# Kernel tuning notes

Hardware: AMD Instinct MI355X
Metric: run time of the kernel (lower is better)

Reference implementation:

```python
import jax, jax.numpy as jnp
import numpy as np

B, N, C = 4, 2048, 384
H = 6
D = C // H
HID = int(C * 4.0)
EPS = 1e-5


def setup_inputs() -> dict:
    key = jax.random.key(0)
    ks = jax.random.split(key, 12)
    s = lambda fan_in: 1.0 / np.sqrt(fan_in)
    return {
        "x": jax.random.normal(ks[0], (B, N, C), dtype=jnp.float32),
        "ln1_g": jnp.ones((C,), jnp.float32),
        "ln1_b": jnp.zeros((C,), jnp.float32),
        "w_qkv": jax.random.uniform(ks[1], (C, 3 * C), jnp.float32, -s(C), s(C)),
        "w_proj": jax.random.uniform(ks[2], (C, C), jnp.float32, -s(C), s(C)),
        "b_proj": jax.random.uniform(ks[3], (C,), jnp.float32, -s(C), s(C)),
        "ln2_g": jnp.ones((C,), jnp.float32),
        "ln2_b": jnp.zeros((C,), jnp.float32),
        "w_fc1": jax.random.uniform(ks[4], (C, HID), jnp.float32, -s(C), s(C)),
        "b_fc1": jax.random.uniform(ks[5], (HID,), jnp.float32, -s(C), s(C)),
        "w_fc2": jax.random.uniform(ks[6], (HID, C), jnp.float32, -s(HID), s(HID)),
        "b_fc2": jax.random.uniform(ks[7], (C,), jnp.float32, -s(HID), s(HID)),
    }


def _layernorm(x, g, b):
    mu = jnp.mean(x, axis=-1, keepdims=True)
    var = jnp.mean(jnp.square(x - mu), axis=-1, keepdims=True)
    return (x - mu) * jax.lax.rsqrt(var + EPS) * g + b


def reference(x, ln1_g, ln1_b, w_qkv, w_proj, b_proj, ln2_g, ln2_b, w_fc1, b_fc1, w_fc2, b_fc2):
    # --- attention branch (pre-norm) ---
    h = _layernorm(x, ln1_g, ln1_b)                       # [B,N,C]
    qkv = (h @ w_qkv).reshape(B, N, 3, H, D)
    q = jnp.transpose(qkv[:, :, 0], (0, 2, 1, 3))          # [B,H,N,D]
    k = jnp.transpose(qkv[:, :, 1], (0, 2, 1, 3))
    v = jnp.transpose(qkv[:, :, 2], (0, 2, 1, 3))
    scale = D ** -0.5
    attn = jnp.einsum("bhnd,bhmd->bhnm", q, k) * scale     # [B,H,N,N]
    attn = jax.nn.softmax(attn, axis=-1)
    o = jnp.einsum("bhnm,bhmd->bhnd", attn, v)             # [B,H,N,D]
    o = jnp.transpose(o, (0, 2, 1, 3)).reshape(B, N, C)
    x = x + (o @ w_proj + b_proj)
    # --- MLP branch (pre-norm) ---
    h2 = _layernorm(x, ln2_g, ln2_b)
    m = jax.nn.gelu(h2 @ w_fc1 + b_fc1, approximate=False)  # torch nn.GELU = exact erf
    x = x + (m @ w_fc2 + b_fc2)
    return x
```

## Files before the change

### kernel.cpp

```cpp
#include <hip/hip_runtime.h>

typedef __bf16 bf16x8 __attribute__((ext_vector_type(8)));
typedef float f32x4 __attribute__((ext_vector_type(4)));
typedef float f32x16 __attribute__((ext_vector_type(16)));
typedef unsigned short u16;
typedef unsigned int u32;
typedef unsigned long long u64;

#define BB 4
#define NNCTX 2048
#define CCH 384
#define NHEAD 6
#define DHEAD 64
#define HIDDIM 1536

__device__ __forceinline__ u16 f2bf(float f){
  u32 u = __builtin_bit_cast(u32, f);
  u = u + 0x7fffu + ((u >> 16) & 1u);
  return (u16)(u >> 16);
}
__device__ __forceinline__ float bf2f(u16 h){
  u32 u = ((u32)h) << 16;
  return __builtin_bit_cast(float, u);
}

union U8 { uint4 u; u16 s[8]; bf16x8 v; };
union F8 { u32 w[4]; bf16x8 v; };

__global__ __launch_bounds__(256) void cast_tr(const float* __restrict__ w0, const float* __restrict__ w1,
    const float* __restrict__ w2, const float* __restrict__ w3,
    u16* __restrict__ o0, u16* __restrict__ o1, u16* __restrict__ o2, u16* __restrict__ o3){
  __shared__ float S[64][65];
  int idx = blockIdx.x;
  const float* src; u16* dst; int K, N, kt, nt;
  if (idx < 108){ src = w0; dst = o0; K = 384; N = 1152; kt = idx / 18; nt = idx % 18; }
  else if (idx < 144){ idx -= 108; src = w1; dst = o1; K = 384; N = 384; kt = idx / 6; nt = idx % 6; }
  else if (idx < 288){ idx -= 144; src = w2; dst = o2; K = 384; N = 1536; kt = idx / 24; nt = idx % 24; }
  else { idx -= 288; src = w3; dst = o3; K = 1536; N = 384; kt = idx / 6; nt = idx % 6; }
  int t = threadIdx.x;
  int r4 = t >> 6, c = t & 63;
  int k0 = kt * 64, n0 = nt * 64;
  #pragma unroll
  for (int i = 0; i < 16; i++){
    int row = i * 4 + r4;
    S[row][c] = src[(size_t)(k0 + row) * N + n0 + c];
  }
  __syncthreads();
  #pragma unroll
  for (int i = 0; i < 16; i++){
    int row = i * 4 + r4;
    dst[(size_t)(n0 + row) * K + k0 + c] = f2bf(S[c][row]);
  }
}

__global__ __launch_bounds__(128) void ln_kernel(const float* __restrict__ x, const float* __restrict__ g,
                                                 const float* __restrict__ bb, u16* __restrict__ out){
  int row = blockIdx.x, t = threadIdx.x;
  const float* xr = x + (size_t)row * CCH;
  float v0 = xr[t], v1 = xr[t + 128], v2 = xr[t + 256];
  float s = v0 + v1 + v2;
  float q = v0 * v0 + v1 * v1 + v2 * v2;
  #pragma unroll
  for (int o = 32; o; o >>= 1){ s += __shfl_down(s, o); q += __shfl_down(q, o); }
  __shared__ float sh[4];
  if ((t & 63) == 0){ int w = t >> 6; sh[w * 2] = s; sh[w * 2 + 1] = q; }
  __syncthreads();
  float sum = sh[0] + sh[2], ssq = sh[1] + sh[3];
  float mu = sum * (1.0f / 384.0f);
  float rstd = rsqrtf(ssq * (1.0f / 384.0f) - mu * mu + 1e-5f);
  size_t base = (size_t)row * CCH;
  out[base + t]       = f2bf((v0 - mu) * rstd * g[t]       + bb[t]);
  out[base + t + 128] = f2bf((v1 - mu) * rstd * g[t + 128] + bb[t + 128]);
  out[base + t + 256] = f2bf((v2 - mu) * rstd * g[t + 256] + bb[t + 256]);
}

template<int EPI, int DBUF>
__global__ __launch_bounds__(256) void gemm_bf16(const u16* __restrict__ A, const u16* __restrict__ Bt,
    int K, int Nn, u16* __restrict__ outb, const float* __restrict__ bias,
    const float* __restrict__ resid, float* __restrict__ outf)
{
  __shared__ u16 As[DBUF + 1][64][68];
  __shared__ u16 Bs[DBUF + 1][64][68];
  int t = threadIdx.x;
  int bm = blockIdx.y * 64, bn = blockIdx.x * 64;
  int l = t & 63, w = t >> 6;
  int wm = (w >> 1) * 32, wn = (w & 1) * 32;
  f32x4 acc[2][2] = {};
  int ar0 = t >> 3, ac0 = (t & 7) * 8;
  uint4 la0, la1, lb0, lb1;
  auto LOADG = [&](int k0){
    la0 = *(const uint4*)&A[(size_t)(bm + ar0) * K + k0 + ac0];
    la1 = *(const uint4*)&A[(size_t)(bm + ar0 + 32) * K + k0 + ac0];
    lb0 = *(const uint4*)&Bt[(size_t)(bn + ar0) * K + k0 + ac0];
    lb1 = *(const uint4*)&Bt[(size_t)(bn + ar0 + 32) * K + k0 + ac0];
  };
  auto WRITEL = [&](int bf){
    *(uint4*)&As[bf][ar0][ac0]      = la0;
    *(uint4*)&As[bf][ar0 + 32][ac0] = la1;
    *(uint4*)&Bs[bf][ar0][ac0]      = lb0;
    *(uint4*)&Bs[bf][ar0 + 32][ac0] = lb1;
  };
  auto COMPUTE = [&](int bf){
    #pragma unroll
    for (int ks = 0; ks < 2; ks++){
      int kb = ks * 32 + (l >> 4) * 8;
      bf16x8 a0  = *(const bf16x8*)&As[bf][wm + (l & 15)][kb];
      bf16x8 a1  = *(const bf16x8*)&As[bf][wm + 16 + (l & 15)][kb];
      bf16x8 bb0 = *(const bf16x8*)&Bs[bf][wn + (l & 15)][kb];
      bf16x8 bb1 = *(const bf16x8*)&Bs[bf][wn + 16 + (l & 15)][kb];
      acc[0][0] = __builtin_amdgcn_mfma_f32_16x16x32_bf16(a0, bb0, acc[0][0], 0, 0, 0);
      acc[0][1] = __builtin_amdgcn_mfma_f32_16x16x32_bf16(a0, bb1, acc[0][1], 0, 0, 0);
      acc[1][0] = __builtin_amdgcn_mfma_f32_16x16x32_bf16(a1, bb0, acc[1][0], 0, 0, 0);
      acc[1][1] = __builtin_amdgcn_mfma_f32_16x16x32_bf16(a1, bb1, acc[1][1], 0, 0, 0);
    }
  };
  if constexpr (DBUF){
    int nk = K >> 6;
    LOADG(0);
    WRITEL(0);
    __syncthreads();
    for (int ki = 0; ki < nk; ki++){
      int cur = ki & 1;
      if (ki + 1 < nk) LOADG((ki + 1) << 6);
      COMPUTE(cur);
      if (ki + 1 < nk) WRITEL(cur ^ 1);
      __syncthreads();
    }
  } else {
    for (int k0 = 0; k0 < K; k0 += 64){
      __syncthreads();
      LOADG(k0);
      WRITEL(0);
      __syncthreads();
      COMPUTE(0);
    }
  }
  if constexpr (EPI == 1){
    #pragma unroll
    for (int mi = 0; mi < 2; mi++)
    #pragma unroll
    for (int ni = 0; ni < 2; ni++)
    #pragma unroll
    for (int r = 0; r < 4; r++){
      int row = bm + wm + mi * 16 + ((l >> 4) << 2) + r;
      int col = bn + wn + ni * 16 + (l & 15);
      size_t idx = (size_t)row * Nn + col;
      outf[idx] = resid[idx] + acc[mi][ni][r] + bias[col];
    }
  } else {
    __syncthreads();
    u16 (*CS)[68] = As[0];
    #pragma unroll
    for (int mi = 0; mi < 2; mi++)
    #pragma unroll
    for (int ni = 0; ni < 2; ni++)
    #pragma unroll
    for (int r = 0; r < 4; r++){
      int row = wm + mi * 16 + ((l >> 4) << 2) + r;
      int col = wn + ni * 16 + (l & 15);
      float v = acc[mi][ni][r];
      if (EPI == 2){
        v += bias[bn + col];
        v = 0.5f * v * (1.0f + erff(v * 0.70710678118f));
      }
      CS[row][col] = f2bf(v);
    }
    __syncthreads();
    int row = t >> 2, c0 = (t & 3) * 16;
    uint4 v0 = *(const uint4*)&CS[row][c0];
    uint4 v1 = *(const uint4*)&CS[row][c0 + 8];
    u16* op = outb + (size_t)(bm + row) * Nn + bn + c0;
    *(uint4*)op       = v0;
    *(uint4*)(op + 8) = v1;
  }
}

#define PVSTEP(O0, O1, O2, O3, SX, BASE, VT)                                     \
  {                                                                              \
    float p0 = __builtin_exp2f(SX[BASE + 0] - m_q);                              \
    float p1 = __builtin_exp2f(SX[BASE + 1] - m_q);                              \
    float p2 = __builtin_exp2f(SX[BASE + 2] - m_q);                              \
    float p3 = __builtin_exp2f(SX[BASE + 3] - m_q);                              \
    float p4 = __builtin_exp2f(SX[BASE + 4] - m_q);                              \
    float p5 = __builtin_exp2f(SX[BASE + 5] - m_q);                              \
    float p6 = __builtin_exp2f(SX[BASE + 6] - m_q);                              \
    float p7 = __builtin_exp2f(SX[BASE + 7] - m_q);                              \
    u32 wa0, wa1, wb0, wb1;                                                      \
    asm("v_cvt_pk_bf16_f32 %0, %1, %2" : "=v"(wa0) : "v"(p0), "v"(p1));          \
    asm("v_cvt_pk_bf16_f32 %0, %1, %2" : "=v"(wa1) : "v"(p2), "v"(p3));          \
    asm("v_cvt_pk_bf16_f32 %0, %1, %2" : "=v"(wb0) : "v"(p4), "v"(p5));          \
    asm("v_cvt_pk_bf16_f32 %0, %1, %2" : "=v"(wb1) : "v"(p6), "v"(p7));          \
    asm("v_permlane32_swap_b32 %0, %1" : "+v"(wa0), "+v"(wb0));                  \
    asm("v_permlane32_swap_b32 %0, %1" : "+v"(wa1), "+v"(wb1));                  \
    F8 pa; pa.w[0] = wa0; pa.w[1] = wa1; pa.w[2] = wb0; pa.w[3] = wb1;           \
    u64 ta, tb, tc, td;                                                          \
    asm volatile("ds_read_b64_tr_b16 %0, %4 offset:" #O0 "\n\t"                  \
                 "ds_read_b64_tr_b16 %1, %4 offset:" #O1 "\n\t"                  \
                 "ds_read_b64_tr_b16 %2, %4 offset:" #O2 "\n\t"                  \
                 "ds_read_b64_tr_b16 %3, %4 offset:" #O3 "\n\t"                  \
                 "s_waitcnt lgkmcnt(0)"                                          \
                 : "=&v"(ta), "=&v"(tb), "=&v"(tc), "=&v"(td)                    \
                 : "v"(VT));                                                     \
    __builtin_amdgcn_sched_barrier(0);                                           \
    F8 f0, f1;                                                                   \
    f0.w[0] = (u32)ta; f0.w[1] = (u32)(ta >> 32);                                \
    f0.w[2] = (u32)tb; f0.w[3] = (u32)(tb >> 32);                                \
    f1.w[0] = (u32)tc; f1.w[1] = (u32)(tc >> 32);                                \
    f1.w[2] = (u32)td; f1.w[3] = (u32)(td >> 32);                                \
    l_acc = __builtin_amdgcn_mfma_f32_32x32x16_bf16(pa.v, onesf, l_acc, 0, 0, 0);\
    o_0 = __builtin_amdgcn_mfma_f32_32x32x16_bf16(pa.v, f0.v, o_0, 0, 0, 0);     \
    o_1 = __builtin_amdgcn_mfma_f32_32x32x16_bf16(pa.v, f1.v, o_1, 0, 0, 0);     \
  }

__global__ __launch_bounds__(256, 3) void attn_mfma(const u16* __restrict__ qkv,
    u16* __restrict__ o0buf, u16* __restrict__ o1buf, float2* __restrict__ mlbuf){
  __shared__ u16 Ks[2][64][68];
  __shared__ __attribute__((aligned(128))) u16 Vs[2][4096];
  int t = threadIdx.x;
  int w = t >> 6, l = t & 63;
  int c31 = l & 31, hi = l >> 5, hi8 = hi * 8;
  int id = blockIdx.x;
  int xcd = id & 7, slot = id >> 3;
  int qb = slot & 15;
  int group = (slot >> 4) * 8 + xcd;
  int bh = group % (BB * NHEAD);
  int sp = group / (BB * NHEAD);
  int b = bh / NHEAD, h = bh % NHEAD;
  int q0 = qb * 128;

  const float QS = 0.1803368801111716f;
  bf16x8 qf[4];
  {
    const u16* qp = qkv + (size_t)(b * NNCTX + q0 + w * 32 + c31) * 1152 + h * 64 + hi8;
    #pragma unroll
    for (int c = 0; c < 4; c++){
      U8 r; r.u = *(const uint4*)(qp + c * 16);
      #pragma unroll
      for (int j = 0; j < 8; j++) r.s[j] = f2bf(bf2f(r.s[j]) * QS);
      qf[c] = r.v;
    }
  }
  bf16x8 onesf;
  {
    U8 r;
    #pragma unroll
    for (int j = 0; j < 8; j++) r.s[j] = 0x3F80;
    onesf = r.v;
  }
  f32x16 o_0 = {}, o_1 = {};
  f32x16 l_acc = {};
  float m_q = -3.4e38f;

  const size_t kvrow = (size_t)(b * NNCTX) * 1152 + h * 64;
  int kkey = t >> 2, kdp = (t & 3) * 16;
  int vkey = t & 63, vdblk = w * 16;
  int voff = (vkey >> 2) * 256 + w * 64 + (vkey & 3) * 16;
  int lg = l >> 4, lr16 = l & 15;
  u32 vtr = (u32)(uintptr_t)(&Vs[0][0]) + (u32)((lg >> 1) * 1024 + (lg & 1) * 128 + lr16 * 8);

  int ktbeg = sp * 16, ktend = ktbeg + 16;
  const u16* kp = qkv + kvrow + (size_t)(ktbeg * 64 + kkey) * 1152 + 384 + kdp;
  const u16* vp = qkv + kvrow + (size_t)(ktbeg * 64 + vkey) * 1152 + 768 + vdblk;
  const int KVSTRIDE = 64 * 1152;

  uint4 kra, krb, vra, vrb;
  auto LOADT = [&](){
    kra = *(const uint4*)kp;
    krb = *(const uint4*)(kp + 8);
    vra = *(const uint4*)vp;
    vrb = *(const uint4*)(vp + 8);
    kp += KVSTRIDE; vp += KVSTRIDE;
  };
  auto WRITET = [&](int bf){
    *(uint4*)&Ks[bf][kkey][kdp]     = kra;
    *(uint4*)&Ks[bf][kkey][kdp + 8] = krb;
    *(uint4*)&Vs[bf][voff]     = vra;
    *(uint4*)&Vs[bf][voff + 8] = vrb;
  };

  LOADT();
  WRITET(0);
  __syncthreads();

  for (int kt = ktbeg; kt < ktend; kt++){
    int cur = (kt - ktbeg) & 1;
    if (kt + 1 < ktend) LOADT();

    f32x16 s0 = {}, s1 = {};
    #pragma unroll
    for (int c = 0; c < 4; c++){
      bf16x8 kf0 = *(const bf16x8*)&Ks[cur][c31][c * 16 + hi8];
      bf16x8 kf1 = *(const bf16x8*)&Ks[cur][32 + c31][c * 16 + hi8];
      s0 = __builtin_amdgcn_mfma_f32_32x32x16_bf16(kf0, qf[c], s0, 0, 0, 0);
      s1 = __builtin_amdgcn_mfma_f32_32x32x16_bf16(kf1, qf[c], s1, 0, 0, 0);
    }
    float tm[16];
    #pragma unroll
    for (int r = 0; r < 16; r++) tm[r] = fmaxf(s0[r], s1[r]);
    #pragma unroll
    for (int st = 8; st >= 1; st >>= 1)
      #pragma unroll
      for (int r = 0; r < st; r++) tm[r] = fmaxf(tm[r], tm[r + st]);
    float px = fmaxf(tm[0], __shfl_xor(tm[0], 32));
    if (!__all(px <= m_q + 8.f)){
      float mn = fmaxf(m_q, px);
      float a = __builtin_exp2f(m_q - mn);
      m_q = mn;
      #pragma unroll
      for (int r = 0; r < 16; r++){
        int cr = (r & 3) + 8 * (r >> 2) + 4 * hi;
        float ar = __shfl(a, cr);
        o_0[r] *= ar; o_1[r] *= ar; l_acc[r] *= ar;
      }
    }
    u32 vt = vtr + (u32)(cur * 8192);
    PVSTEP(0, 512, 256, 768, s0, 0, vt)
    PVSTEP(2048, 2560, 2304, 2816, s0, 8, vt)
    PVSTEP(4096, 4608, 4352, 4864, s1, 0, vt)
    PVSTEP(6144, 6656, 6400, 6912, s1, 8, vt)

    if (kt + 1 < ktend) WRITET(cur ^ 1);
    __syncthreads();
  }
  u16* obuf = sp ? o1buf : o0buf;
  #pragma unroll
  for (int r = 0; r < 16; r++){
    int cr = (r & 3) + 8 * (r >> 2) + 4 * hi;
    float mr = __shfl(m_q, cr);
    int n = q0 + w * 32 + cr;
    size_t row = (size_t)(b * NNCTX + n);
    u16* op = obuf + row * CCH + h * 64;
    op[c31]      = f2bf(o_0[r]);
    op[32 + c31] = f2bf(o_1[r]);
    if (c31 == 0)
      mlbuf[((size_t)(sp * BB * NHEAD + bh)) * NNCTX + n] = make_float2(mr, l_acc[r]);
  }
}

__global__ __launch_bounds__(256) void attn_combine(u16* __restrict__ o0, const u16* __restrict__ o1,
    const float2* __restrict__ ml){
  int g = blockIdx.x * 256 + threadIdx.x;
  int row = g / 48, c8 = g - row * 48;
  int head = c8 >> 3;
  int b = row >> 11, n = row & 2047;
  int bh = b * NHEAD + head;
  float2 a = ml[(size_t)bh * NNCTX + n];
  float2 c = ml[(size_t)(BB * NHEAD + bh) * NNCTX + n];
  float M = fmaxf(a.x, c.x);
  float e0 = exp2f(a.x - M), e1 = exp2f(c.x - M);
  float inv = 1.0f / (a.y * e0 + c.y * e1);
  float s0 = e0 * inv, s1 = e1 * inv;
  size_t idx = (size_t)row * CCH + c8 * 8;
  U8 x0, x1, o;
  x0.u = *(const uint4*)(o0 + idx);
  x1.u = *(const uint4*)(o1 + idx);
  #pragma unroll
  for (int j = 0; j < 8; j++) o.s[j] = f2bf(bf2f(x0.s[j]) * s0 + bf2f(x1.s[j]) * s1);
  *(uint4*)(o0 + idx) = o.u;
}

extern "C" void kernel_launch(void* const* d_in, const int* in_sizes, int n_in,
                              void* d_out, int out_size, void* d_ws, size_t ws_size,
                              hipStream_t stream){
  const float* x      = (const float*)d_in[0];
  const float* ln1_g  = (const float*)d_in[1];
  const float* ln1_b  = (const float*)d_in[2];
  const float* w_qkv  = (const float*)d_in[3];
  const float* w_proj = (const float*)d_in[4];
  const float* b_proj = (const float*)d_in[5];
  const float* ln2_g  = (const float*)d_in[6];
  const float* ln2_b  = (const float*)d_in[7];
  const float* w_fc1  = (const float*)d_in[8];
  const float* b_fc1  = (const float*)d_in[9];
  const float* w_fc2  = (const float*)d_in[10];
  const float* b_fc2  = (const float*)d_in[11];
  float* out = (float*)d_out;

  u16* ws = (u16*)d_ws;
  u16* wqkv_bf  = ws;
  u16* wproj_bf = wqkv_bf + 442368;
  u16* wfc1_bf  = wproj_bf + 147456;
  u16* wfc2_bf  = wfc1_bf + 589824;
  u16* h_bf     = wfc2_bf + 589824;
  u16* qkv_bf   = h_bf + 3145728;
  u16* opart1   = qkv_bf + 9437184;
  float2* mlbuf = (float2*)(opart1 + 3145728);
  u16* opart0   = h_bf;
  u16* m_bf     = qkv_bf;

  cast_tr<<<432, 256, 0, stream>>>(w_qkv, w_proj, w_fc1, w_fc2, wqkv_bf, wproj_bf, wfc1_bf, wfc2_bf);

  ln_kernel<<<8192, 128, 0, stream>>>(x, ln1_g, ln1_b, h_bf);
  gemm_bf16<0, 0><<<dim3(18, 128), 256, 0, stream>>>(h_bf, wqkv_bf, 384, 1152, qkv_bf, nullptr, nullptr, nullptr);
  attn_mfma<<<dim3(768), 256, 0, stream>>>(qkv_bf, opart0, opart1, mlbuf);
  attn_combine<<<1536, 256, 0, stream>>>(opart0, opart1, mlbuf);
  gemm_bf16<1, 1><<<dim3(6, 128), 256, 0, stream>>>(opart0, wproj_bf, 384, 384, nullptr, b_proj, x, out);
  ln_kernel<<<8192, 128, 0, stream>>>(out, ln2_g, ln2_b, h_bf);
  gemm_bf16<2, 0><<<dim3(24, 128), 256, 0, stream>>>(h_bf, wfc1_bf, 384, 1536, m_bf, b_fc1, nullptr, nullptr);
  gemm_bf16<1, 1><<<dim3(6, 128), 256, 0, stream>>>(m_bf, wfc2_bf, 1536, 384, nullptr, b_fc2, out, out);
}
```

Before: 155.9 us.

## Add 128x128-tile GEMM with direct global-to-LDS loads for QKV and FC1

Adds a new bf16 MFMA GEMM kernel that uses 128x128 output tiles, a 4x4 MFMA fragment grid per wave, and global_load_lds async copies into double-buffered shared memory. The QKV and FC1 GEMMs switch to it. The larger tiles raise operand reuse and cut global traffic per FLOP, and the direct-to-LDS loads skip staging through registers. The epilogue writes through LDS for coalesced 16-byte stores. Risks are fewer blocks, higher register pressure, and LDS bank conflicts on the unpadded 32-wide rows.

```diff
diff --git a/kernel.cpp b/kernel.cpp
--- a/kernel.cpp
+++ b/kernel.cpp
@@ -26,6 +26,11 @@
 
 union U8 { uint4 u; u16 s[8]; bf16x8 v; };
 union F8 { u32 w[4]; bf16x8 v; };
+
+__device__ __forceinline__ void gl_lds16(const u16* g, u16* l){
+  __builtin_amdgcn_global_load_lds((const __attribute__((address_space(1))) u32*)g,
+                                   (__attribute__((address_space(3))) u32*)l, 16, 0, 0);
+}
 
 __global__ __launch_bounds__(256) void cast_tr(const float* __restrict__ w0, const float* __restrict__ w1,
     const float* __restrict__ w2, const float* __restrict__ w3,
@@ -72,6 +77,72 @@
   out[base + t]       = f2bf((v0 - mu) * rstd * g[t]       + bb[t]);
   out[base + t + 128] = f2bf((v1 - mu) * rstd * g[t + 128] + bb[t + 128]);
   out[base + t + 256] = f2bf((v2 - mu) * rstd * g[t + 256] + bb[t + 256]);
+}
+
+template<int EPI>
+__global__ __launch_bounds__(256) void gemm128(const u16* __restrict__ A, const u16* __restrict__ Bt,
+    int K, int Nn, u16* __restrict__ outb, const float* __restrict__ bias)
+{
+  __shared__ u16 L[16384];
+  int t = threadIdx.x;
+  int bm = blockIdx.y * 128, bn = blockIdx.x * 128;
+  int l = t & 63, w = t >> 6;
+  int wm = (w >> 1) * 64, wn = (w & 1) * 64;
+  int lr = l & 15, lg = l >> 4;
+  f32x4 acc[4][4] = {};
+  int srow = t >> 2, scol = (t & 3) * 8;
+  auto STAGE = [&](int bf, int k0){
+    #pragma unroll
+    for (int i = 0; i < 2; i++){
+      int row = srow + i * 64;
+      gl_lds16(&A[(size_t)(bm + row) * K + k0 + scol],  &L[bf * 8192 + (t + i * 256) * 8]);
+      gl_lds16(&Bt[(size_t)(bn + row) * K + k0 + scol], &L[bf * 8192 + 4096 + (t + i * 256) * 8]);
+    }
+  };
+  auto COMPUTE = [&](int bf){
+    bf16x8 af[4], bfr[4];
+    #pragma unroll
+    for (int mi = 0; mi < 4; mi++) af[mi] = *(const bf16x8*)&L[bf * 8192 + (wm + mi * 16 + lr) * 32 + lg * 8];
+    #pragma unroll
+    for (int ni = 0; ni < 4; ni++) bfr[ni] = *(const bf16x8*)&L[bf * 8192 + 4096 + (wn + ni * 16 + lr) * 32 + lg * 8];
+    #pragma unroll
+    for (int mi = 0; mi < 4; mi++)
+      #pragma unroll
+      for (int ni = 0; ni < 4; ni++)
+        acc[mi][ni] = __builtin_amdgcn_mfma_f32_16x16x32_bf16(af[mi], bfr[ni], acc[mi][ni], 0, 0, 0);
+  };
+  int nk = K >> 5;
+  STAGE(0, 0);
+  __syncthreads();
+  for (int ki = 0; ki < nk; ki++){
+    int cur = ki & 1;
+    if (ki + 1 < nk) STAGE(cur ^ 1, (ki + 1) << 5);
+    COMPUTE(cur);
+    __syncthreads();
+  }
+  #pragma unroll
+  for (int mi = 0; mi < 4; mi++)
+  #pragma unroll
+  for (int ni = 0; ni < 4; ni++)
+  #pragma unroll
+  for (int r = 0; r < 4; r++){
+    int row = wm + mi * 16 + lg * 4 + r;
+    int col = wn + ni * 16 + lr;
+    float v = acc[mi][ni][r];
+    if (EPI == 2){
+      v += bias[bn + col];
+      v = 0.5f * v * (1.0f + erff(v * 0.70710678118f));
+    }
+    L[row * 128 + col] = f2bf(v);
+  }
+  __syncthreads();
+  {
+    int row = t >> 1, colh = (t & 1) * 64;
+    const uint4* src = (const uint4*)&L[row * 128 + colh];
+    uint4* dst = (uint4*)(outb + (size_t)(bm + row) * Nn + bn + colh);
+    #pragma unroll
+    for (int i = 0; i < 8; i++) dst[i] = src[i];
+  }
 }
 
 template<int EPI, int DBUF>
@@ -391,11 +462,11 @@
   cast_tr<<<432, 256, 0, stream>>>(w_qkv, w_proj, w_fc1, w_fc2, wqkv_bf, wproj_bf, wfc1_bf, wfc2_bf);
 
   ln_kernel<<<8192, 128, 0, stream>>>(x, ln1_g, ln1_b, h_bf);
-  gemm_bf16<0, 0><<<dim3(18, 128), 256, 0, stream>>>(h_bf, wqkv_bf, 384, 1152, qkv_bf, nullptr, nullptr, nullptr);
+  gemm128<0><<<dim3(9, 64), 256, 0, stream>>>(h_bf, wqkv_bf, 384, 1152, qkv_bf, nullptr);
   attn_mfma<<<dim3(768), 256, 0, stream>>>(qkv_bf, opart0, opart1, mlbuf);
   attn_combine<<<1536, 256, 0, stream>>>(opart0, opart1, mlbuf);
   gemm_bf16<1, 1><<<dim3(6, 128), 256, 0, stream>>>(opart0, wproj_bf, 384, 384, nullptr, b_proj, x, out);
   ln_kernel<<<8192, 128, 0, stream>>>(out, ln2_g, ln2_b, h_bf);
-  gemm_bf16<2, 0><<<dim3(24, 128), 256, 0, stream>>>(h_bf, wfc1_bf, 384, 1536, m_bf, b_fc1, nullptr, nullptr);
+  gemm128<2><<<dim3(12, 64), 256, 0, stream>>>(h_bf, wfc1_bf, 384, 1536, m_bf, b_fc1);
   gemm_bf16<1, 1><<<dim3(6, 128), 256, 0, stream>>>(m_bf, wfc2_bf, 1536, 384, nullptr, b_fc2, out, out);
 }
```

Result: slower. 163.0 us (+4.6%).
